# Performance work log

Measured on AMD Instinct MI355X. Metric: run time of the kernel, lower is better.

## Reference

```python
import jax, jax.numpy as jnp
import numpy as np

B, NX, NY, NZ = 2, 64, 64, 64
D, CI, CO, F = 3, 32, 32, 64  # spatial dims, chan in/out, n_modes


def setup_inputs() -> dict:
    key = jax.random.key(0)
    ka, kx, ky, k1, k2, k3, k4, k5, k6 = jax.random.split(key, 9)
    omega, c = 30.0 / 300.0, 6.0
    u = lambda k, shape, scale: scale * (2.0 * jax.random.uniform(k, shape, jnp.float32) - 1.0)
    return {
        "a": jax.random.normal(ka, (B, NX, NY, NZ, CI), jnp.float32),
        "x": jax.random.uniform(kx, (B, NX, NY, NZ, D), jnp.float32),
        "y": jax.random.uniform(ky, (B, NX, NY, NZ, D), jnp.float32),
        "modes_a": u(k1, (F, CI), np.sqrt(c / (CI + F))),
        "modes_x": u(k2, (F, D), np.sqrt(c / (D + F)) * omega),
        "modes_y": u(k3, (F, D), np.sqrt(c / (D + F)) * omega),
        "modes_u": u(k4, (F, CO), np.sqrt(c / (F + CO))),
        "fc_w": jax.random.normal(k5, (CI, CO), jnp.float32) / np.sqrt(CI),
        "fc_b": jax.random.normal(k6, (CO,), jnp.float32) * 0.01,
    }


def reference(a, x, y, modes_a, modes_x, modes_y, modes_u, fc_w, fc_b):
    # SpectralAttention: Fourier-feature linear attention.
    # NOTE: source forward passes x for both coordinate args (att(h, x, x)).
    A = jnp.einsum('bxyzi,fi->bxyzf', a, modes_a)                       # [B,NX,NY,NZ,F]
    X = jnp.exp(-2j * np.pi * jnp.einsum('bxyzd,gd->bxyzg', x, modes_x))  # complex64
    Y = jnp.exp(2j * np.pi * jnp.einsum('bxyzd,gd->bxyzg', x, modes_y))   # complex64
    N = x.shape[1] * x.shape[2] * x.shape[3]
    AX = jnp.einsum('bxyzf,bxyzg->bfg', A.astype(X.dtype), X)           # [B,F,F] complex
    U = jnp.einsum('bfg,bxyzg->bxyzf', AX, Y).real / N                  # [B,NX,NY,NZ,F]
    u = jnp.einsum('bxyzf,fo->bxyzo', U, modes_u)                        # [B,NX,NY,NZ,CO]
    h = u + a @ fc_w + fc_b                                              # residual Linear
    return jax.nn.gelu(h)
```

## Files before the change

kernel.cpp:

```cpp
#include <hip/hip_runtime.h>
#include <math.h>

#define NB   2
#define NPTS 262144

typedef __attribute__((ext_vector_type(8))) __bf16 bf16x8;
typedef __attribute__((ext_vector_type(4))) float  f32x4;

__device__ __forceinline__ float gelu_fast(float v) {
    float t  = v * v;
    float z2 = v * (-2.302208f + -0.1029432f * t);
    float e  = __builtin_amdgcn_exp2f(z2);
    return v * __builtin_amdgcn_rcpf(1.0f + e);
}

__device__ __forceinline__ unsigned short bf16_rn(float f) {
    unsigned u = __builtin_bit_cast(unsigned, f);
    u += 0x7fffu + ((u >> 16) & 1u);
    return (unsigned short)(u >> 16);
}

template<bool WRITE_ABF>
__global__ __launch_bounds__(256)
void pass1_kernel(const float* __restrict__ a, const float* __restrict__ x,
                  const float* __restrict__ mx, float* __restrict__ part,
                  unsigned* __restrict__ abf, int NPB)
{
    __shared__ float4 xs[4][32];
    __shared__ float wsum[32 * 129];
    __shared__ __align__(16) float atile[4][1024];

    const int t = threadIdx.x, wave = t >> 6, lane = t & 63;
    const int l15 = lane & 15, l4 = lane >> 4;
    const int blk = blockIdx.x, b = blk / NPB, pb = blk % NPB;
    const int ppb = NPTS / NPB;
    const int chunks = ppb >> 5;
    const long base = (long)b * NPTS + (long)pb * ppb;

    float m0[4], m1[4], m2[4];
    #pragma unroll
    for (int ct = 0; ct < 4; ++ct) {
        int g = l15 + 16 * ct;
        m0[ct] = mx[g*3]; m1[ct] = mx[g*3+1]; m2[ct] = mx[g*3+2];
    }

    f32x4 acc[2][8];
    #pragma unroll
    for (int rt = 0; rt < 2; ++rt)
        #pragma unroll
        for (int ct = 0; ct < 8; ++ct)
            acc[rt][ct] = f32x4{0.f, 0.f, 0.f, 0.f};

    for (int ci = wave; ci < chunks; ci += 4) {
        const long pc = base + ((long)ci << 5);

        if (lane < 32) {
            const float* xq = x + (pc + lane) * 3;
            xs[wave][lane] = make_float4(xq[0], xq[1], xq[2], 0.f);
        }
        #pragma unroll
        for (int q = 0; q < 4; ++q) {
            float4 v = *(const float4*)(a + pc * 32 + q * 256 + lane * 4);
            *(float4*)&atile[wave][q * 256 + lane * 4] = v;
        }

        bf16x8 afr[2];
        #pragma unroll
        for (int j = 0; j < 8; ++j) {
            float2 av = *(const float2*)&atile[wave][(l4*8 + j) * 32 + 2*l15];
            unsigned short h0 = bf16_rn(av.x);
            unsigned short h1 = bf16_rn(av.y);
            if (WRITE_ABF)
                abf[(pc + l4*8 + j) * 16 + l15] = (unsigned)h0 | ((unsigned)h1 << 16);
            afr[0][j] = __builtin_bit_cast(__bf16, h0);
            afr[1][j] = __builtin_bit_cast(__bf16, h1);
        }

        float4 xp[8];
        #pragma unroll
        for (int j = 0; j < 8; ++j) xp[j] = xs[wave][l4*8 + j];

        #pragma unroll
        for (int ct = 0; ct < 4; ++ct) {
            bf16x8 bc, bs;
            #pragma unroll
            for (int j = 0; j < 8; ++j) {
                float d = xp[j].x*m0[ct] + xp[j].y*m1[ct] + xp[j].z*m2[ct];
                bc[j] = (__bf16)__builtin_amdgcn_cosf(d);
                bs[j] = (__bf16)__builtin_amdgcn_sinf(d);
            }
            #pragma unroll
            for (int rt = 0; rt < 2; ++rt) {
                acc[rt][ct]   = __builtin_amdgcn_mfma_f32_16x16x32_bf16(afr[rt], bc, acc[rt][ct],   0, 0, 0);
                acc[rt][ct+4] = __builtin_amdgcn_mfma_f32_16x16x32_bf16(afr[rt], bs, acc[rt][ct+4], 0, 0, 0);
            }
        }
    }

    for (int w = 0; w < 4; ++w) {
        if (wave == w) {
            #pragma unroll
            for (int rt = 0; rt < 2; ++rt)
                #pragma unroll
                for (int ct = 0; ct < 8; ++ct)
                    #pragma unroll
                    for (int r = 0; r < 4; ++r) {
                        int i = 2 * (l4*4 + r) + rt;
                        int c = ((ct & 3) * 16) + l15 + ((ct & 4) ? 64 : 0);
                        int id = i * 129 + c;
                        float v = acc[rt][ct][r];
                        if (w == 0) wsum[id] = v; else wsum[id] += v;
                    }
        }
        __syncthreads();
    }
    for (int idx = t; idx < 4096; idx += 256) {
        int i = idx >> 7, c = idx & 127;
        part[(long)blk * 4096 + idx] = wsum[i * 129 + c];
    }
}

__global__ __launch_bounds__(256)
void reduceW_kernel(const float* __restrict__ part, float* __restrict__ Wf, int NPB)
{
    __shared__ float red[8][33];
    const int t = threadIdx.x;
    const int b = blockIdx.x >> 7;
    const int jb = (blockIdx.x & 127) * 32;
    const int jj = jb + (t & 31), seg = t >> 5;
    const float* p = part + (long)b * NPB * 4096 + jj;
    float s = 0.f;
    for (int pb = seg; pb < NPB; pb += 8) s += p[(long)pb * 4096];
    red[seg][t & 31] = s;
    __syncthreads();
    if (t < 32) {
        float r = 0.f;
        #pragma unroll
        for (int q = 0; q < 8; ++q) r += red[q][t];
        Wf[b * 4096 + jb + t] = r;
    }
}

__global__ __launch_bounds__(256)
void vmat_kernel(const float* __restrict__ Wf, const float* __restrict__ ma,
                 const float* __restrict__ mu, const float* __restrict__ fcw,
                 unsigned short* __restrict__ Vb)
{
    __shared__ float Ws[4096];
    __shared__ float Qs[32][32];
    const int t = threadIdx.x, b = blockIdx.x;
    for (int i = t; i < 4096; i += 256) Ws[i] = Wf[b * 4096 + i];
    __syncthreads();
    for (int i = t; i < 1024; i += 256) {
        int o = i >> 5, ii = i & 31;
        float s = 0.f;
        for (int f = 0; f < 64; ++f) s += mu[f*32 + o] * ma[f*32 + ii];
        Qs[o][ii] = s;
    }
    __syncthreads();
    const float invN = 1.f / 262144.f;
    for (int i = t; i < 5120; i += 256) {
        int k = i >> 5, o = i & 31;
        float v;
        if (k < 128) {
            int g = k & 63, off = (k >= 64) ? 64 : 0;
            float s = 0.f;
            for (int q = 0; q < 32; ++q) s += Qs[o][q] * Ws[q*128 + off + g];
            v = s * invN;
        } else {
            v = fcw[(k - 128) * 32 + o];
        }
        Vb[b * 5120 + i] = bf16_rn(v);
    }
}

template<bool READ_ABF>
__global__ __launch_bounds__(256)
void pass2_kernel(const float* __restrict__ a, const unsigned* __restrict__ abf,
                  const float* __restrict__ x, const unsigned short* __restrict__ Vb,
                  const float* __restrict__ fcb, const float* __restrict__ my,
                  float* __restrict__ out)
{
    __shared__ float4 xs[4][32];
    __shared__ float4 mys[64];
    __shared__ __align__(16) float st[4][16][32];
    const int t = threadIdx.x, wave = t >> 6, lane = t & 63;
    const int l15 = lane & 15, l4 = lane >> 4;
    const int blk = blockIdx.x, b = blk >> 9, lb = blk & 511;
    const long base = (long)b * NPTS + (long)lb * 512;

    if (t < 64) { const float* mq = my + t*3; mys[t] = make_float4(mq[0], mq[1], mq[2], 0.f); }

    bf16x8 bfr[5][2];
    {
        const unsigned short* vb = Vb + b * 5120;
        #pragma unroll
        for (int c = 0; c < 5; ++c)
            #pragma unroll
            for (int ct = 0; ct < 2; ++ct) {
                bf16x8 tmp;
                #pragma unroll
                for (int j = 0; j < 8; ++j) {
                    unsigned short uv = vb[(32*c + l4*8 + j) * 32 + l15 + 16*ct];
                    tmp[j] = __builtin_bit_cast(__bf16, uv);
                }
                bfr[c][ct] = tmp;
            }
    }
    const float bias0 = fcb[l15], bias1 = fcb[l15 + 16];
    __syncthreads();

    {
        const long p0 = base + ((long)wave << 5);
        if (lane < 32) {
            const float* xq = x + (p0 + lane) * 3;
            xs[wave][lane] = make_float4(xq[0], xq[1], xq[2], 0.f);
        }
    }
    bf16x8 afr[2];
    {
        const long p0 = base + ((long)wave << 5);
        #pragma unroll
        for (int rt = 0; rt < 2; ++rt) {
            if (READ_ABF) {
                afr[rt] = __builtin_bit_cast(bf16x8,
                    *(const uint4*)(abf + (p0 + l15 + 16*rt) * 16 + l4*4));
            } else {
                const float* ap = a + (p0 + l15 + 16*rt) * 32 + l4*8;
                float4 a0 = *(const float4*)ap;
                float4 a1 = *(const float4*)(ap + 4);
                afr[rt][0] = (__bf16)a0.x; afr[rt][1] = (__bf16)a0.y;
                afr[rt][2] = (__bf16)a0.z; afr[rt][3] = (__bf16)a0.w;
                afr[rt][4] = (__bf16)a1.x; afr[rt][5] = (__bf16)a1.y;
                afr[rt][6] = (__bf16)a1.z; afr[rt][7] = (__bf16)a1.w;
            }
        }
    }

    for (int ci = wave; ci < 16; ci += 4) {
        const long pc = base + ((long)ci << 5);
        const bool hasnext = (ci + 4) < 16;
        const long pn = base + ((long)(ci + 4) << 5);

        float4 xp0 = xs[wave][l15];
        float4 xp1 = xs[wave][l15 + 16];

        bf16x8 anfr[2];
        if (hasnext) {
            #pragma unroll
            for (int rt = 0; rt < 2; ++rt) {
                if (READ_ABF) {
                    anfr[rt] = __builtin_bit_cast(bf16x8,
                        *(const uint4*)(abf + (pn + l15 + 16*rt) * 16 + l4*4));
                } else {
                    const float* ap = a + (pn + l15 + 16*rt) * 32 + l4*8;
                    float4 a0 = *(const float4*)ap;
                    float4 a1 = *(const float4*)(ap + 4);
                    anfr[rt][0] = (__bf16)a0.x; anfr[rt][1] = (__bf16)a0.y;
                    anfr[rt][2] = (__bf16)a0.z; anfr[rt][3] = (__bf16)a0.w;
                    anfr[rt][4] = (__bf16)a1.x; anfr[rt][5] = (__bf16)a1.y;
                    anfr[rt][6] = (__bf16)a1.z; anfr[rt][7] = (__bf16)a1.w;
                }
            }
            if (lane < 32) {
                const float* xq = x + (pn + lane) * 3;
                xs[wave][lane] = make_float4(xq[0], xq[1], xq[2], 0.f);
            }
        }

        f32x4 acc[2][2];
        #pragma unroll
        for (int rt = 0; rt < 2; ++rt)
            #pragma unroll
            for (int ct = 0; ct < 2; ++ct) acc[rt][ct] = f32x4{0.f,0.f,0.f,0.f};

        #pragma unroll
        for (int gt = 0; gt < 2; ++gt) {
            bf16x8 ac[2], as2[2];
            #pragma unroll
            for (int j = 0; j < 8; ++j) {
                float4 m = mys[gt*32 + l4*8 + j];
                float d0 = xp0.x*m.x + xp0.y*m.y + xp0.z*m.z;
                float d1 = xp1.x*m.x + xp1.y*m.y + xp1.z*m.z;
                ac[0][j]  = (__bf16)__builtin_amdgcn_cosf(d0);
                as2[0][j] = (__bf16)__builtin_amdgcn_sinf(d0);
                ac[1][j]  = (__bf16)__builtin_amdgcn_cosf(d1);
                as2[1][j] = (__bf16)__builtin_amdgcn_sinf(d1);
            }
            #pragma unroll
            for (int rt = 0; rt < 2; ++rt)
                #pragma unroll
                for (int ct = 0; ct < 2; ++ct) {
                    acc[rt][ct] = __builtin_amdgcn_mfma_f32_16x16x32_bf16(ac[rt],  bfr[gt][ct],   acc[rt][ct], 0, 0, 0);
                    acc[rt][ct] = __builtin_amdgcn_mfma_f32_16x16x32_bf16(as2[rt], bfr[2+gt][ct], acc[rt][ct], 0, 0, 0);
                }
        }
        #pragma unroll
        for (int rt = 0; rt < 2; ++rt) {
            #pragma unroll
            for (int ct = 0; ct < 2; ++ct) {
                acc[rt][ct] = __builtin_amdgcn_mfma_f32_16x16x32_bf16(afr[rt], bfr[4][ct], acc[rt][ct], 0, 0, 0);
                float bias = ct ? bias1 : bias0;
                #pragma unroll
                for (int r = 0; r < 4; ++r)
                    st[wave][l4*4 + r][l15 + 16*ct] = gelu_fast(acc[rt][ct][r] + bias);
            }
            {
                int row = lane >> 3;
                int c4  = (lane & 7) * 4;
                float4 v0 = *(const float4*)&st[wave][row][c4];
                float4 v1 = *(const float4*)&st[wave][row + 8][c4];
                *(float4*)&out[(pc + 16*rt + row) * 32 + c4]     = v0;
                *(float4*)&out[(pc + 16*rt + row + 8) * 32 + c4] = v1;
            }
        }

        if (hasnext) { afr[0] = anfr[0]; afr[1] = anfr[1]; }
    }
}

extern "C" void kernel_launch(void* const* d_in, const int* in_sizes, int n_in,
                              void* d_out, int out_size, void* d_ws, size_t ws_size,
                              hipStream_t stream)
{
    const float* a   = (const float*)d_in[0];
    const float* x   = (const float*)d_in[1];
    const float* ma  = (const float*)d_in[3];
    const float* mx  = (const float*)d_in[4];
    const float* my  = (const float*)d_in[5];
    const float* mu  = (const float*)d_in[6];
    const float* fcw = (const float*)d_in[7];
    const float* fcb = (const float*)d_in[8];
    float* out = (float*)d_out;

    const size_t WfB  = (size_t)NB * 4096 * 4;
    const size_t VbB  = (size_t)NB * 5120 * 2;
    const size_t abfB = (size_t)NB * NPTS * 16 * 4;

    int NPB = 256;
    bool use_abf = ws_size >= (size_t)NB * NPB * 4096 * 4 + WfB + VbB + abfB + 256;
    if (!use_abf) {
        while (NPB > 32 &&
               ws_size < (size_t)NB * NPB * 4096 * 4 + WfB + VbB + 256)
            NPB >>= 1;
    }

    float* part = (float*)d_ws;
    float* Wf = part + (size_t)NB * NPB * 4096;
    unsigned short* Vb = (unsigned short*)(Wf + NB * 4096);
    unsigned* abf = (unsigned*)(Vb + NB * 5120);

    if (use_abf)
        pass1_kernel<true><<<NB * NPB, 256, 0, stream>>>(a, x, mx, part, abf, NPB);
    else
        pass1_kernel<false><<<NB * NPB, 256, 0, stream>>>(a, x, mx, part, abf, NPB);

    reduceW_kernel<<<NB * 128, 256, 0, stream>>>(part, Wf, NPB);
    vmat_kernel<<<NB, 256, 0, stream>>>(Wf, ma, mu, fcw, Vb);

    if (use_abf)
        pass2_kernel<true><<<NB * 512, 256, 0, stream>>>(a, abf, x, Vb, fcb, my, out);
    else
        pass2_kernel<false><<<NB * 512, 256, 0, stream>>>(a, abf, x, Vb, fcb, my, out);
}
```

Measured before the change: 82.31 us.

## Fuse four-kernel pipeline into one cooperative kernel with grid syncs

Replaces the sequence of pass1, reduce, vmat and pass2 launches with a single cooperative kernel of 512 blocks that uses grid.sync between phases, removing launch gaps and inter-kernel drains. The fallback path keeps the original multi-kernel sequence, and pass2's software prefetch of the next chunk is dropped there. The cost is that the vmat phase runs on only two blocks while all others wait at the grid barrier, grid syncs have their own overhead, and the fused kernel's register pressure and LDS use may lower occupancy.

```diff
diff --git a/kernel.cpp b/kernel.cpp
--- a/kernel.cpp
+++ b/kernel.cpp
@@ -1,5 +1,8 @@
 #include <hip/hip_runtime.h>
+#include <hip/hip_cooperative_groups.h>
 #include <math.h>
+
+namespace cg = cooperative_groups;
 
 #define NB   2
 #define NPTS 262144
@@ -18,6 +21,255 @@
     unsigned u = __builtin_bit_cast(unsigned, f);
     u += 0x7fffu + ((u >> 16) & 1u);
     return (unsigned short)(u >> 16);
+}
+
+__global__ __launch_bounds__(256)
+void fused_kernel(const float* __restrict__ a, const float* __restrict__ x,
+                  const float* __restrict__ mx, const float* __restrict__ my,
+                  const float* __restrict__ ma, const float* __restrict__ mu,
+                  const float* __restrict__ fcw, const float* __restrict__ fcb,
+                  float* __restrict__ part, float* __restrict__ Wf,
+                  unsigned short* __restrict__ Vb, unsigned* __restrict__ abf,
+                  float* __restrict__ out)
+{
+    cg::grid_group grid = cg::this_grid();
+    __shared__ __align__(16) float smem[8736];
+
+    const int t = threadIdx.x, wave = t >> 6, lane = t & 63;
+    const int l15 = lane & 15, l4 = lane >> 4;
+    const int blk = blockIdx.x;
+    const int b = blk >> 8, pb = blk & 255;
+    const long base = (long)b * NPTS + (long)pb * 1024;
+    const int chunks = 32;
+
+    {
+        float4* xs   = (float4*)smem;
+        float* wsum  = smem + 512;
+        float* atile = smem + 4640;
+
+        float m0[4], m1[4], m2[4];
+        #pragma unroll
+        for (int ct = 0; ct < 4; ++ct) {
+            int g = l15 + 16 * ct;
+            m0[ct] = mx[g*3]; m1[ct] = mx[g*3+1]; m2[ct] = mx[g*3+2];
+        }
+
+        f32x4 acc[2][8];
+        #pragma unroll
+        for (int rt = 0; rt < 2; ++rt)
+            #pragma unroll
+            for (int ct = 0; ct < 8; ++ct)
+                acc[rt][ct] = f32x4{0.f, 0.f, 0.f, 0.f};
+
+        for (int ci = wave; ci < chunks; ci += 4) {
+            const long pc = base + ((long)ci << 5);
+
+            if (lane < 32) {
+                const float* xq = x + (pc + lane) * 3;
+                xs[wave*32 + lane] = make_float4(xq[0], xq[1], xq[2], 0.f);
+            }
+            #pragma unroll
+            for (int q = 0; q < 4; ++q) {
+                float4 v = *(const float4*)(a + pc * 32 + q * 256 + lane * 4);
+                *(float4*)&atile[wave*1024 + q * 256 + lane * 4] = v;
+            }
+
+            bf16x8 afr[2];
+            #pragma unroll
+            for (int j = 0; j < 8; ++j) {
+                float2 av = *(const float2*)&atile[wave*1024 + (l4*8 + j) * 32 + 2*l15];
+                unsigned short h0 = bf16_rn(av.x);
+                unsigned short h1 = bf16_rn(av.y);
+                abf[(pc + l4*8 + j) * 16 + l15] = (unsigned)h0 | ((unsigned)h1 << 16);
+                afr[0][j] = __builtin_bit_cast(__bf16, h0);
+                afr[1][j] = __builtin_bit_cast(__bf16, h1);
+            }
+
+            float4 xp[8];
+            #pragma unroll
+            for (int j = 0; j < 8; ++j) xp[j] = xs[wave*32 + l4*8 + j];
+
+            #pragma unroll
+            for (int ct = 0; ct < 4; ++ct) {
+                bf16x8 bc, bs;
+                #pragma unroll
+                for (int j = 0; j < 8; ++j) {
+                    float d = xp[j].x*m0[ct] + xp[j].y*m1[ct] + xp[j].z*m2[ct];
+                    bc[j] = (__bf16)__builtin_amdgcn_cosf(d);
+                    bs[j] = (__bf16)__builtin_amdgcn_sinf(d);
+                }
+                #pragma unroll
+                for (int rt = 0; rt < 2; ++rt) {
+                    acc[rt][ct]   = __builtin_amdgcn_mfma_f32_16x16x32_bf16(afr[rt], bc, acc[rt][ct],   0, 0, 0);
+                    acc[rt][ct+4] = __builtin_amdgcn_mfma_f32_16x16x32_bf16(afr[rt], bs, acc[rt][ct+4], 0, 0, 0);
+                }
+            }
+        }
+
+        for (int w = 0; w < 4; ++w) {
+            if (wave == w) {
+                #pragma unroll
+                for (int rt = 0; rt < 2; ++rt)
+                    #pragma unroll
+                    for (int ct = 0; ct < 8; ++ct)
+                        #pragma unroll
+                        for (int r = 0; r < 4; ++r) {
+                            int i = 2 * (l4*4 + r) + rt;
+                            int c = ((ct & 3) * 16) + l15 + ((ct & 4) ? 64 : 0);
+                            int id = i * 129 + c;
+                            float v = acc[rt][ct][r];
+                            if (w == 0) wsum[id] = v; else wsum[id] += v;
+                        }
+            }
+            __syncthreads();
+        }
+        for (int idx = t; idx < 4096; idx += 256) {
+            int i = idx >> 7, c = idx & 127;
+            part[(long)blk * 4096 + idx] = wsum[i * 129 + c];
+        }
+    }
+    grid.sync();
+
+    {
+        float* red = smem;
+        const int jo = t & 15, seg = t >> 4;
+        const int bb = blk >> 8;
+        const int jb = (blk & 255) * 16;
+        const int jj = jb + jo;
+        const float* p = part + (long)bb * 256 * 4096 + jj;
+        float s = 0.f;
+        #pragma unroll
+        for (int r = 0; r < 16; ++r) s += p[(long)(seg + (r << 4)) * 4096];
+        red[seg * 17 + jo] = s;
+        __syncthreads();
+        if (t < 16) {
+            float r2 = 0.f;
+            #pragma unroll
+            for (int q = 0; q < 16; ++q) r2 += red[q * 17 + t];
+            Wf[bb * 4096 + jb + t] = r2;
+        }
+    }
+    grid.sync();
+
+    if (blk < NB) {
+        float* Ws = smem;
+        float* Qs = smem + 4096;
+        for (int i = t; i < 4096; i += 256) Ws[i] = Wf[blk * 4096 + i];
+        __syncthreads();
+        for (int i = t; i < 1024; i += 256) {
+            int o = i >> 5, ii = i & 31;
+            float s = 0.f;
+            for (int f = 0; f < 64; ++f) s += mu[f*32 + o] * ma[f*32 + ii];
+            Qs[i] = s;
+        }
+        __syncthreads();
+        const float invN = 1.f / 262144.f;
+        for (int i = t; i < 5120; i += 256) {
+            int k = i >> 5, o = i & 31;
+            float v;
+            if (k < 128) {
+                int g = k & 63, off = (k >= 64) ? 64 : 0;
+                float s = 0.f;
+                for (int q = 0; q < 32; ++q) s += Qs[o*32 + q] * Ws[q*128 + off + g];
+                v = s * invN;
+            } else {
+                v = fcw[(k - 128) * 32 + o];
+            }
+            Vb[blk * 5120 + i] = bf16_rn(v);
+        }
+    }
+    grid.sync();
+
+    {
+        float4* xs  = (float4*)smem;
+        float4* mys = (float4*)(smem + 512);
+        float*  st  = smem + 768;
+
+        if (t < 64) { const float* mq = my + t*3; mys[t] = make_float4(mq[0], mq[1], mq[2], 0.f); }
+
+        bf16x8 bfr[5][2];
+        {
+            const unsigned short* vb = Vb + b * 5120;
+            #pragma unroll
+            for (int c = 0; c < 5; ++c)
+                #pragma unroll
+                for (int ct = 0; ct < 2; ++ct) {
+                    bf16x8 tmp;
+                    #pragma unroll
+                    for (int j = 0; j < 8; ++j) {
+                        unsigned short uv = vb[(32*c + l4*8 + j) * 32 + l15 + 16*ct];
+                        tmp[j] = __builtin_bit_cast(__bf16, uv);
+                    }
+                    bfr[c][ct] = tmp;
+                }
+        }
+        const float bias0 = fcb[l15], bias1 = fcb[l15 + 16];
+        __syncthreads();
+
+        for (int ci = wave; ci < chunks; ci += 4) {
+            const long pc = base + ((long)ci << 5);
+
+            if (lane < 32) {
+                const float* xq = x + (pc + lane) * 3;
+                xs[wave*32 + lane] = make_float4(xq[0], xq[1], xq[2], 0.f);
+            }
+            bf16x8 afr[2];
+            #pragma unroll
+            for (int rt = 0; rt < 2; ++rt)
+                afr[rt] = __builtin_bit_cast(bf16x8,
+                    *(const uint4*)(abf + (pc + l15 + 16*rt) * 16 + l4*4));
+
+            float4 xp0 = xs[wave*32 + l15];
+            float4 xp1 = xs[wave*32 + l15 + 16];
+
+            f32x4 acc[2][2];
+            #pragma unroll
+            for (int rt = 0; rt < 2; ++rt)
+                #pragma unroll
+                for (int ct = 0; ct < 2; ++ct) acc[rt][ct] = f32x4{0.f,0.f,0.f,0.f};
+
+            #pragma unroll
+            for (int gt = 0; gt < 2; ++gt) {
+                bf16x8 ac[2], as2[2];
+                #pragma unroll
+                for (int j = 0; j < 8; ++j) {
+                    float4 m = mys[gt*32 + l4*8 + j];
+                    float d0 = xp0.x*m.x + xp0.y*m.y + xp0.z*m.z;
+                    float d1 = xp1.x*m.x + xp1.y*m.y + xp1.z*m.z;
+                    ac[0][j]  = (__bf16)__builtin_amdgcn_cosf(d0);
+                    as2[0][j] = (__bf16)__builtin_amdgcn_sinf(d0);
+                    ac[1][j]  = (__bf16)__builtin_amdgcn_cosf(d1);
+                    as2[1][j] = (__bf16)__builtin_amdgcn_sinf(d1);
+                }
+                #pragma unroll
+                for (int rt = 0; rt < 2; ++rt)
+                    #pragma unroll
+                    for (int ct = 0; ct < 2; ++ct) {
+                        acc[rt][ct] = __builtin_amdgcn_mfma_f32_16x16x32_bf16(ac[rt],  bfr[gt][ct],   acc[rt][ct], 0, 0, 0);
+                        acc[rt][ct] = __builtin_amdgcn_mfma_f32_16x16x32_bf16(as2[rt], bfr[2+gt][ct], acc[rt][ct], 0, 0, 0);
+                    }
+            }
+            #pragma unroll
+            for (int rt = 0; rt < 2; ++rt) {
+                #pragma unroll
+                for (int ct = 0; ct < 2; ++ct) {
+                    acc[rt][ct] = __builtin_amdgcn_mfma_f32_16x16x32_bf16(afr[rt], bfr[4][ct], acc[rt][ct], 0, 0, 0);
+                    float bias = ct ? bias1 : bias0;
+                    #pragma unroll
+                    for (int r = 0; r < 4; ++r)
+                        st[wave*512 + (l4*4 + r)*32 + l15 + 16*ct] = gelu_fast(acc[rt][ct][r] + bias);
+                }
+                {
+                    int row = lane >> 3;
+                    int c4  = (lane & 7) * 4;
+                    float4 v0 = *(const float4*)&st[wave*512 + row*32 + c4];
+                    float4 v1 = *(const float4*)&st[wave*512 + (row + 8)*32 + c4];
+                    *(float4*)&out[(pc + 16*rt + row) * 32 + c4]     = v0;
+                    *(float4*)&out[(pc + 16*rt + row + 8) * 32 + c4] = v1;
+                }
+            }
+        }
+    }
 }
 
 template<bool WRITE_ABF>
@@ -53,7 +305,6 @@
 
     for (int ci = wave; ci < chunks; ci += 4) {
         const long pc = base + ((long)ci << 5);
-
         if (lane < 32) {
             const float* xq = x + (pc + lane) * 3;
             xs[wave][lane] = make_float4(xq[0], xq[1], xq[2], 0.f);
@@ -63,7 +314,6 @@
             float4 v = *(const float4*)(a + pc * 32 + q * 256 + lane * 4);
             *(float4*)&atile[wave][q * 256 + lane * 4] = v;
         }
-
         bf16x8 afr[2];
         #pragma unroll
         for (int j = 0; j < 8; ++j) {
@@ -75,11 +325,9 @@
             afr[0][j] = __builtin_bit_cast(__bf16, h0);
             afr[1][j] = __builtin_bit_cast(__bf16, h1);
         }
-
         float4 xp[8];
         #pragma unroll
         for (int j = 0; j < 8; ++j) xp[j] = xs[wave][l4*8 + j];
-
         #pragma unroll
         for (int ct = 0; ct < 4; ++ct) {
             bf16x8 bc, bs;
@@ -210,23 +458,21 @@
     const float bias0 = fcb[l15], bias1 = fcb[l15 + 16];
     __syncthreads();
 
-    {
-        const long p0 = base + ((long)wave << 5);
+    for (int ci = wave; ci < 16; ci += 4) {
+        const long pc = base + ((long)ci << 5);
+
         if (lane < 32) {
-            const float* xq = x + (p0 + lane) * 3;
+            const float* xq = x + (pc + lane) * 3;
             xs[wave][lane] = make_float4(xq[0], xq[1], xq[2], 0.f);
         }
-    }
-    bf16x8 afr[2];
-    {
-        const long p0 = base + ((long)wave << 5);
+        bf16x8 afr[2];
         #pragma unroll
         for (int rt = 0; rt < 2; ++rt) {
             if (READ_ABF) {
                 afr[rt] = __builtin_bit_cast(bf16x8,
-                    *(const uint4*)(abf + (p0 + l15 + 16*rt) * 16 + l4*4));
+                    *(const uint4*)(abf + (pc + l15 + 16*rt) * 16 + l4*4));
             } else {
-                const float* ap = a + (p0 + l15 + 16*rt) * 32 + l4*8;
+                const float* ap = a + (pc + l15 + 16*rt) * 32 + l4*8;
                 float4 a0 = *(const float4*)ap;
                 float4 a1 = *(const float4*)(ap + 4);
                 afr[rt][0] = (__bf16)a0.x; afr[rt][1] = (__bf16)a0.y;
@@ -235,38 +481,9 @@
                 afr[rt][6] = (__bf16)a1.z; afr[rt][7] = (__bf16)a1.w;
             }
         }
-    }
-
-    for (int ci = wave; ci < 16; ci += 4) {
-        const long pc = base + ((long)ci << 5);
-        const bool hasnext = (ci + 4) < 16;
-        const long pn = base + ((long)(ci + 4) << 5);
 
         float4 xp0 = xs[wave][l15];
         float4 xp1 = xs[wave][l15 + 16];
-
-        bf16x8 anfr[2];
-        if (hasnext) {
-            #pragma unroll
-            for (int rt = 0; rt < 2; ++rt) {
-                if (READ_ABF) {
-                    anfr[rt] = __builtin_bit_cast(bf16x8,
-                        *(const uint4*)(abf + (pn + l15 + 16*rt) * 16 + l4*4));
-                } else {
-                    const float* ap = a + (pn + l15 + 16*rt) * 32 + l4*8;
-                    float4 a0 = *(const float4*)ap;
-                    float4 a1 = *(const float4*)(ap + 4);
-                    anfr[rt][0] = (__bf16)a0.x; anfr[rt][1] = (__bf16)a0.y;
-                    anfr[rt][2] = (__bf16)a0.z; anfr[rt][3] = (__bf16)a0.w;
-                    anfr[rt][4] = (__bf16)a1.x; anfr[rt][5] = (__bf16)a1.y;
-                    anfr[rt][6] = (__bf16)a1.z; anfr[rt][7] = (__bf16)a1.w;
-                }
-            }
-            if (lane < 32) {
-                const float* xq = x + (pn + lane) * 3;
-                xs[wave][lane] = make_float4(xq[0], xq[1], xq[2], 0.f);
-            }
-        }
 
         f32x4 acc[2][2];
         #pragma unroll
@@ -314,8 +531,6 @@
                 *(float4*)&out[(pc + 16*rt + row + 8) * 32 + c4] = v1;
             }
         }
-
-        if (hasnext) { afr[0] = anfr[0]; afr[1] = anfr[1]; }
     }
 }
 
@@ -333,33 +548,43 @@
     const float* fcb = (const float*)d_in[8];
     float* out = (float*)d_out;
 
-    const size_t WfB  = (size_t)NB * 4096 * 4;
-    const size_t VbB  = (size_t)NB * 5120 * 2;
-    const size_t abfB = (size_t)NB * NPTS * 16 * 4;
-
-    int NPB = 256;
-    bool use_abf = ws_size >= (size_t)NB * NPB * 4096 * 4 + WfB + VbB + abfB + 256;
-    if (!use_abf) {
-        while (NPB > 32 &&
-               ws_size < (size_t)NB * NPB * 4096 * 4 + WfB + VbB + 256)
-            NPB >>= 1;
-    }
-
+    const int NPB = 256;
     float* part = (float*)d_ws;
     float* Wf = part + (size_t)NB * NPB * 4096;
     unsigned short* Vb = (unsigned short*)(Wf + NB * 4096);
     unsigned* abf = (unsigned*)(Vb + NB * 5120);
 
-    if (use_abf)
-        pass1_kernel<true><<<NB * NPB, 256, 0, stream>>>(a, x, mx, part, abf, NPB);
-    else
-        pass1_kernel<false><<<NB * NPB, 256, 0, stream>>>(a, x, mx, part, abf, NPB);
-
-    reduceW_kernel<<<NB * 128, 256, 0, stream>>>(part, Wf, NPB);
-    vmat_kernel<<<NB, 256, 0, stream>>>(Wf, ma, mu, fcw, Vb);
-
-    if (use_abf)
-        pass2_kernel<true><<<NB * 512, 256, 0, stream>>>(a, abf, x, Vb, fcb, my, out);
-    else
-        pass2_kernel<false><<<NB * 512, 256, 0, stream>>>(a, abf, x, Vb, fcb, my, out);
-}
+    const size_t needB = ((size_t)NB * NPB * 4096 + NB * 4096) * 4
+                       + (size_t)NB * 5120 * 2 + (size_t)NB * NPTS * 16 * 4 + 256;
+    bool fits = ws_size >= needB;
+
+    hipError_t cerr = hipErrorUnknown;
+    if (fits) {
+        int dev = 0;
+        hipGetDevice(&dev);
+        int coop = 0;
+        hipDeviceGetAttribute(&coop, hipDeviceAttributeCooperativeLaunch, dev);
+        if (coop) {
+            void* args[] = {
+                (void*)&a, (void*)&x, (void*)&mx, (void*)&my, (void*)&ma,
+                (void*)&mu, (void*)&fcw, (void*)&fcb, (void*)&part, (void*)&Wf,
+                (void*)&Vb, (void*)&abf, (void*)&out
+            };
+            cerr = hipLaunchCooperativeKernel((const void*)fused_kernel,
+                                              dim3(512), dim3(256), args, 0, stream);
+        }
+    }
+    if (cerr != hipSuccess) {
+        if (fits) {
+            pass1_kernel<true><<<NB * NPB, 256, 0, stream>>>(a, x, mx, part, abf, NPB);
+            reduceW_kernel<<<NB * 128, 256, 0, stream>>>(part, Wf, NPB);
+            vmat_kernel<<<NB, 256, 0, stream>>>(Wf, ma, mu, fcw, Vb);
+            pass2_kernel<true><<<NB * 512, 256, 0, stream>>>(a, abf, x, Vb, fcb, my, out);
+        } else {
+            pass1_kernel<false><<<NB * NPB, 256, 0, stream>>>(a, x, mx, part, abf, NPB);
+            reduceW_kernel<<<NB * 128, 256, 0, stream>>>(part, Wf, NPB);
+            vmat_kernel<<<NB, 256, 0, stream>>>(Wf, ma, mu, fcw, Vb);
+            pass2_kernel<false><<<NB * 512, 256, 0, stream>>>(a, abf, x, Vb, fcb, my, out);
+        }
+    }
+}
```

Measured after the change: 243.4 us. 2.96x slower.
